# Optimization experiments

Measured on AMD Instinct MI355X. Metric: run time of the kernel, lower is better.

The kernel has to match this reference:

```python
import jax, jax.numpy as jnp
import numpy as np

B, L, D, V = 64, 512, 768, 100
LN_EPS = 1e-6


def setup_inputs() -> dict:
    key = jax.random.key(0)
    k1, k2, k3, k4 = jax.random.split(key, 4)
    return {
        "ids": jax.random.randint(k1, (B, 1), 0, V),
        "pooler": jax.random.normal(k2, (B, L, D), dtype=jnp.float32),
        "emb_table": jax.random.normal(k3, (V, 2), dtype=jnp.float32),
        "W_dense": jax.random.normal(k4, (2, D), dtype=jnp.float32) * 0.1,
        "b_dense": jnp.zeros((D,), dtype=jnp.float32),
        "gamma": jnp.ones((D,), dtype=jnp.float32),
        "beta": jnp.zeros((D,), dtype=jnp.float32),
    }


def reference(ids, pooler, emb_table, W_dense, b_dense, gamma, beta):
    # id -> 2-dim projection -> dense to embed_dim: xt (B, 1, D)
    emb = emb_table[ids]                      # (B, 1, 2)
    xt = emb @ W_dense + b_dense              # (B, 1, D)

    # Per timestep i the original concatenates [pooler[:, i], xt] into a
    # 2-token sequence and runs dot-product self-attention (keras Attention,
    # no scaling), then sums over the 2 tokens. Vectorized over all L steps:
    tok = jnp.stack([pooler, jnp.broadcast_to(xt, pooler.shape)], axis=2)  # (B, L, 2, D)
    scores = jnp.einsum('blqd,blkd->blqk', tok, tok)                       # (B, L, 2, 2)
    attn = jax.nn.softmax(scores, axis=-1)
    out = jnp.einsum('blqk,blkd->blqd', attn, tok)                         # (B, L, 2, D)
    summed = out.sum(axis=2)                                               # (B, L, D)

    # dropout is identity at inference; layernorm over last axis, eps=1e-6
    mean = summed.mean(axis=-1, keepdims=True)
    var = summed.var(axis=-1, keepdims=True)
    normed = (summed - mean) * jax.lax.rsqrt(var + LN_EPS)
    return normed * gamma + beta
```

## Files before the change

kernel.cpp:

```cpp
#include <hip/hip_runtime.h>


constexpr int Bc = 64;
constexpr int Lc = 512;
constexpr int Dc = 768;
constexpr float LN_EPS = 1e-6f;
constexpr int WAVES_PER_BLOCK = 4;

typedef float nv_float4 __attribute__((ext_vector_type(4)));

__global__ __launch_bounds__(64 * WAVES_PER_BLOCK) void hier_attn_ln_kernel(
    const int*   __restrict__ ids,
    const float* __restrict__ pooler,
    const float* __restrict__ emb_table,
    const float* __restrict__ W,
    const float* __restrict__ bvec,
    const float* __restrict__ gamma,
    const float* __restrict__ beta,
    float*       __restrict__ out)
{
    const int wave = threadIdx.x >> 6;
    const int lane = threadIdx.x & 63;
    const int row  = blockIdx.x * WAVES_PER_BLOCK + wave;
    const int b    = row >> 9;

    const float4* prow4 = (const float4*)(pooler + (size_t)row * Dc);
    nv_float4*    orow4 = (nv_float4*)(out + (size_t)row * Dc);
    const float4* W0_4  = (const float4*)W;
    const float4* W1_4  = (const float4*)(W + Dc);
    const float4* b_4   = (const float4*)bvec;
    const float4* g_4   = (const float4*)gamma;
    const float4* be_4  = (const float4*)beta;

    const int id = ids[b];
    const float e0 = emb_table[id * 2 + 0];
    const float e1 = emb_table[id * 2 + 1];

    float4 t0[3], t1[3];
    float s00 = 0.f, s01 = 0.f, s11 = 0.f, S0 = 0.f, S1 = 0.f;

#pragma unroll
    for (int j = 0; j < 3; ++j) {
        const int idx4 = lane + j * 64;
        float4 p  = prow4[idx4];
        float4 w0 = W0_4[idx4];
        float4 w1 = W1_4[idx4];
        float4 bd = b_4[idx4];
        float4 x;
        x.x = fmaf(e0, w0.x, fmaf(e1, w1.x, bd.x));
        x.y = fmaf(e0, w0.y, fmaf(e1, w1.y, bd.y));
        x.z = fmaf(e0, w0.z, fmaf(e1, w1.z, bd.z));
        x.w = fmaf(e0, w0.w, fmaf(e1, w1.w, bd.w));
        t0[j] = p;
        t1[j] = x;
        s00 += p.x*p.x + p.y*p.y + p.z*p.z + p.w*p.w;
        s01 += p.x*x.x + p.y*x.y + p.z*x.z + p.w*x.w;
        s11 += x.x*x.x + x.y*x.y + x.z*x.z + x.w*x.w;
        S0  += p.x + p.y + p.z + p.w;
        S1  += x.x + x.y + x.z + x.w;
    }

#pragma unroll
    for (int off = 32; off > 0; off >>= 1) {
        s00 += __shfl_xor(s00, off);
        s01 += __shfl_xor(s01, off);
        s11 += __shfl_xor(s11, off);
        S0  += __shfl_xor(S0,  off);
        S1  += __shfl_xor(S1,  off);
    }

    const float m0  = fmaxf(s00, s01);
    const float a00 = __expf(s00 - m0);
    const float a01 = __expf(s01 - m0);
    const float r0  = 1.f / (a00 + a01);
    const float m1  = fmaxf(s01, s11);
    const float a10 = __expf(s01 - m1);
    const float a11 = __expf(s11 - m1);
    const float r1  = 1.f / (a10 + a11);
    const float w0s = a00 * r0 + a10 * r1;
    const float w1s = a01 * r0 + a11 * r1;

    const float invD = 1.f / (float)Dc;
    const float mean = (w0s * S0 + w1s * S1) * invD;
    const float ex2  = (w0s*w0s*s00 + 2.f*w0s*w1s*s01 + w1s*w1s*s11) * invD;
    const float var  = ex2 - mean * mean;
    const float rstd = rsqrtf(var + LN_EPS);

#pragma unroll
    for (int j = 0; j < 3; ++j) {
        const int idx4 = lane + j * 64;
        float4 gm = g_4[idx4];
        float4 bt = be_4[idx4];
        nv_float4 o;
        o.x = (fmaf(w0s, t0[j].x, w1s * t1[j].x) - mean) * rstd * gm.x + bt.x;
        o.y = (fmaf(w0s, t0[j].y, w1s * t1[j].y) - mean) * rstd * gm.y + bt.y;
        o.z = (fmaf(w0s, t0[j].z, w1s * t1[j].z) - mean) * rstd * gm.z + bt.z;
        o.w = (fmaf(w0s, t0[j].w, w1s * t1[j].w) - mean) * rstd * gm.w + bt.w;
        __builtin_nontemporal_store(o, &orow4[idx4]);
    }
}

extern "C" void kernel_launch(void* const* d_in, const int* in_sizes, int n_in,
                              void* d_out, int out_size, void* d_ws, size_t ws_size,
                              hipStream_t stream) {
    const int*   ids       = (const int*)  d_in[0];
    const float* pooler    = (const float*)d_in[1];
    const float* emb_table = (const float*)d_in[2];
    const float* W_dense   = (const float*)d_in[3];
    const float* b_dense   = (const float*)d_in[4];
    const float* gamma     = (const float*)d_in[5];
    const float* beta      = (const float*)d_in[6];
    float* out = (float*)d_out;

    const int nrows = Bc * Lc;
    hipLaunchKernelGGL(hier_attn_ln_kernel,
                       dim3(nrows / WAVES_PER_BLOCK), dim3(64 * WAVES_PER_BLOCK),
                       0, stream,
                       ids, pooler, emb_table, W_dense, b_dense, gamma, beta, out);
}
```

Before: 187.2 us.

## Process multiple rows per wave with reused projections and next-row prefetch

Each wave now handles eight consecutive rows instead of one. The projected xt vector, its self-dot and sum, and gamma/beta are computed or loaded once per wave and reused for all eight rows. The next row's pooler data is prefetched with nontemporal loads while the current row is reduced and written. This cuts redundant parameter loads and per-row setup, but it launches far fewer waves, which can reduce the memory-level parallelism available to hide latency.

```diff
diff --git a/kernel.cpp b/kernel.cpp
--- a/kernel.cpp
+++ b/kernel.cpp
@@ -6,6 +6,7 @@
 constexpr int Dc = 768;
 constexpr float LN_EPS = 1e-6f;
 constexpr int WAVES_PER_BLOCK = 4;
+constexpr int ROWS_PER_WAVE = 8;
 
 typedef float nv_float4 __attribute__((ext_vector_type(4)));
 
@@ -21,82 +22,101 @@
 {
     const int wave = threadIdx.x >> 6;
     const int lane = threadIdx.x & 63;
-    const int row  = blockIdx.x * WAVES_PER_BLOCK + wave;
-    const int b    = row >> 9;
-
-    const float4* prow4 = (const float4*)(pooler + (size_t)row * Dc);
-    nv_float4*    orow4 = (nv_float4*)(out + (size_t)row * Dc);
-    const float4* W0_4  = (const float4*)W;
-    const float4* W1_4  = (const float4*)(W + Dc);
-    const float4* b_4   = (const float4*)bvec;
-    const float4* g_4   = (const float4*)gamma;
-    const float4* be_4  = (const float4*)beta;
+    const int row0 = (blockIdx.x * WAVES_PER_BLOCK + wave) * ROWS_PER_WAVE;
+    const int b    = row0 >> 9;
 
     const int id = ids[b];
     const float e0 = emb_table[id * 2 + 0];
     const float e1 = emb_table[id * 2 + 1];
 
-    float4 t0[3], t1[3];
-    float s00 = 0.f, s01 = 0.f, s11 = 0.f, S0 = 0.f, S1 = 0.f;
-
+    float4 xt[3], gm[3], bt[3];
+    float s11 = 0.f, S1 = 0.f;
 #pragma unroll
     for (int j = 0; j < 3; ++j) {
         const int idx4 = lane + j * 64;
-        float4 p  = prow4[idx4];
-        float4 w0 = W0_4[idx4];
-        float4 w1 = W1_4[idx4];
-        float4 bd = b_4[idx4];
+        float4 w0 = ((const float4*)W)[idx4];
+        float4 w1 = ((const float4*)(W + Dc))[idx4];
+        float4 bd = ((const float4*)bvec)[idx4];
         float4 x;
         x.x = fmaf(e0, w0.x, fmaf(e1, w1.x, bd.x));
         x.y = fmaf(e0, w0.y, fmaf(e1, w1.y, bd.y));
         x.z = fmaf(e0, w0.z, fmaf(e1, w1.z, bd.z));
         x.w = fmaf(e0, w0.w, fmaf(e1, w1.w, bd.w));
-        t0[j] = p;
-        t1[j] = x;
-        s00 += p.x*p.x + p.y*p.y + p.z*p.z + p.w*p.w;
-        s01 += p.x*x.x + p.y*x.y + p.z*x.z + p.w*x.w;
+        xt[j] = x;
+        gm[j] = ((const float4*)gamma)[idx4];
+        bt[j] = ((const float4*)beta)[idx4];
         s11 += x.x*x.x + x.y*x.y + x.z*x.z + x.w*x.w;
-        S0  += p.x + p.y + p.z + p.w;
         S1  += x.x + x.y + x.z + x.w;
     }
-
 #pragma unroll
     for (int off = 32; off > 0; off >>= 1) {
-        s00 += __shfl_xor(s00, off);
-        s01 += __shfl_xor(s01, off);
         s11 += __shfl_xor(s11, off);
-        S0  += __shfl_xor(S0,  off);
         S1  += __shfl_xor(S1,  off);
     }
 
-    const float m0  = fmaxf(s00, s01);
-    const float a00 = __expf(s00 - m0);
-    const float a01 = __expf(s01 - m0);
-    const float r0  = 1.f / (a00 + a01);
-    const float m1  = fmaxf(s01, s11);
-    const float a10 = __expf(s01 - m1);
-    const float a11 = __expf(s11 - m1);
-    const float r1  = 1.f / (a10 + a11);
-    const float w0s = a00 * r0 + a10 * r1;
-    const float w1s = a01 * r0 + a11 * r1;
+    const nv_float4* prow4 = (const nv_float4*)(pooler + (size_t)row0 * Dc);
+    nv_float4*       orow4 = (nv_float4*)(out + (size_t)row0 * Dc);
+    const float invD = 1.f / (float)Dc;
 
-    const float invD = 1.f / (float)Dc;
-    const float mean = (w0s * S0 + w1s * S1) * invD;
-    const float ex2  = (w0s*w0s*s00 + 2.f*w0s*w1s*s01 + w1s*w1s*s11) * invD;
-    const float var  = ex2 - mean * mean;
-    const float rstd = rsqrtf(var + LN_EPS);
+    float4 pn[3];
+#pragma unroll
+    for (int j = 0; j < 3; ++j) {
+        nv_float4 t = __builtin_nontemporal_load(&prow4[lane + j * 64]);
+        pn[j] = make_float4(t.x, t.y, t.z, t.w);
+    }
+
+    for (int r = 0; r < ROWS_PER_WAVE; ++r) {
+        float4 p[3];
+#pragma unroll
+        for (int j = 0; j < 3; ++j) p[j] = pn[j];
+        if (r + 1 < ROWS_PER_WAVE) {
+#pragma unroll
+            for (int j = 0; j < 3; ++j) {
+                nv_float4 t = __builtin_nontemporal_load(
+                    &prow4[(size_t)(r + 1) * 192 + lane + j * 64]);
+                pn[j] = make_float4(t.x, t.y, t.z, t.w);
+            }
+        }
+
+        float s00 = 0.f, s01 = 0.f, S0 = 0.f;
+#pragma unroll
+        for (int j = 0; j < 3; ++j) {
+            s00 += p[j].x*p[j].x  + p[j].y*p[j].y  + p[j].z*p[j].z  + p[j].w*p[j].w;
+            s01 += p[j].x*xt[j].x + p[j].y*xt[j].y + p[j].z*xt[j].z + p[j].w*xt[j].w;
+            S0  += p[j].x + p[j].y + p[j].z + p[j].w;
+        }
+#pragma unroll
+        for (int off = 32; off > 0; off >>= 1) {
+            s00 += __shfl_xor(s00, off);
+            s01 += __shfl_xor(s01, off);
+            S0  += __shfl_xor(S0,  off);
+        }
+
+        const float m0  = fmaxf(s00, s01);
+        const float a00 = __expf(s00 - m0);
+        const float a01 = __expf(s01 - m0);
+        const float r0  = 1.f / (a00 + a01);
+        const float m1  = fmaxf(s01, s11);
+        const float a10 = __expf(s01 - m1);
+        const float a11 = __expf(s11 - m1);
+        const float r1  = 1.f / (a10 + a11);
+        const float w0s = a00 * r0 + a10 * r1;
+        const float w1s = a01 * r0 + a11 * r1;
+
+        const float mean = (w0s * S0 + w1s * S1) * invD;
+        const float ex2  = (w0s*w0s*s00 + 2.f*w0s*w1s*s01 + w1s*w1s*s11) * invD;
+        const float var  = ex2 - mean * mean;
+        const float rstd = rsqrtf(var + LN_EPS);
 
 #pragma unroll
-    for (int j = 0; j < 3; ++j) {
-        const int idx4 = lane + j * 64;
-        float4 gm = g_4[idx4];
-        float4 bt = be_4[idx4];
-        nv_float4 o;
-        o.x = (fmaf(w0s, t0[j].x, w1s * t1[j].x) - mean) * rstd * gm.x + bt.x;
-        o.y = (fmaf(w0s, t0[j].y, w1s * t1[j].y) - mean) * rstd * gm.y + bt.y;
-        o.z = (fmaf(w0s, t0[j].z, w1s * t1[j].z) - mean) * rstd * gm.z + bt.z;
-        o.w = (fmaf(w0s, t0[j].w, w1s * t1[j].w) - mean) * rstd * gm.w + bt.w;
-        __builtin_nontemporal_store(o, &orow4[idx4]);
+        for (int j = 0; j < 3; ++j) {
+            nv_float4 o;
+            o.x = (fmaf(w0s, p[j].x, w1s * xt[j].x) - mean) * rstd * gm[j].x + bt[j].x;
+            o.y = (fmaf(w0s, p[j].y, w1s * xt[j].y) - mean) * rstd * gm[j].y + bt[j].y;
+            o.z = (fmaf(w0s, p[j].z, w1s * xt[j].z) - mean) * rstd * gm[j].z + bt[j].z;
+            o.w = (fmaf(w0s, p[j].w, w1s * xt[j].w) - mean) * rstd * gm[j].w + bt[j].w;
+            __builtin_nontemporal_store(o, &orow4[(size_t)r * 192 + lane + j * 64]);
+        }
     }
 }
 
@@ -112,9 +132,10 @@
     const float* beta      = (const float*)d_in[6];
     float* out = (float*)d_out;
 
-    const int nrows = Bc * Lc;
+    const int nrows  = Bc * Lc;
+    const int blocks = nrows / (WAVES_PER_BLOCK * ROWS_PER_WAVE);
     hipLaunchKernelGGL(hier_attn_ln_kernel,
-                       dim3(nrows / WAVES_PER_BLOCK), dim3(64 * WAVES_PER_BLOCK),
+                       dim3(blocks), dim3(64 * WAVES_PER_BLOCK),
                        0, stream,
                        ids, pooler, emb_table, W_dense, b_dense, gamma, beta, out);
 }
```

New measurement: 189.0 us. About the same (+0.9%).
